# Performance work log

Measured on AMD Instinct MI355X. Metric: run time of the kernel, lower is better.

## Reference

```python
import jax, jax.numpy as jnp
import numpy as np

# ShiftedSteSign forward: binary sign (0 -> +1). STE only matters for backward.

def ste_sign(x):
    return jnp.where(x >= 0, 1.0, -1.0).astype(x.dtype)

N, D, U, E = 32768, 1024, 1024, 3  # tokens, d_in, units, kernel_estimators


def setup_inputs() -> dict:
    key = jax.random.key(0)
    kx, k0, k1, k2 = jax.random.split(key, 4)
    x = jax.random.normal(kx, (N, D), dtype=jnp.float32)
    # keras 'random_uniform' initializer default range [-0.05, 0.05]
    kernels = [jax.random.uniform(k, (D, U), jnp.float32, -0.05, 0.05) for k in (k0, k1, k2)]
    # alpha initialized as ||kernel||_1 along axis 0 divided by d_in (trainable)
    alphas = [jnp.sum(jnp.abs(kw), axis=0) / D for kw in kernels]
    return {"x": x,
            "k0": kernels[0], "k1": kernels[1], "k2": kernels[2],
            "a0": alphas[0], "a1": alphas[1], "a2": alphas[2]}


def reference(x, k0, k1, k2, a0, a1, a2):
    d = x.shape[-1]
    xq = ste_sign(x)                                   # [N, D] binary
    beta = jnp.sum(jnp.abs(x), axis=-1) / d            # [N]
    out = jnp.zeros((x.shape[0], k0.shape[1]), x.dtype)
    for kw, a in ((k0, a0), (k1, a1), (k2, a2)):
        Z = xq @ ste_sign(kw)                          # binary GEMM [N, U]
        out = out + Z * (beta[:, None] * a[None, :])   # outer-product scale
    return out
```

## Files before the change

### kernel.cpp

```cpp
#include <hip/hip_runtime.h>
#include <hip/hip_bf16.h>
#include <stdint.h>

#define N_TOK 32768
#define D_IN  1024
#define U_OUT 1024

typedef __attribute__((ext_vector_type(8))) short short8;
typedef __attribute__((ext_vector_type(4))) float f32x4;

__device__ __forceinline__ void async_copy16(const void* g, void* l) {
  __builtin_amdgcn_global_load_lds(
      (const __attribute__((address_space(1))) void*)g,
      (__attribute__((address_space(3))) void*)l,
      16, 0, 0);
}

__global__ __launch_bounds__(256) void quant_kernel(
    const float* __restrict__ x,
    unsigned short* __restrict__ xq,
    float* __restrict__ beta) {
  const int row = blockIdx.x;
  const int tid = threadIdx.x;
  const float4 v = ((const float4*)(x + (size_t)row * D_IN))[tid];

  ushort4 s;
  s.x = (v.x >= 0.f) ? 0x3F80u : 0xBF80u;
  s.y = (v.y >= 0.f) ? 0x3F80u : 0xBF80u;
  s.z = (v.z >= 0.f) ? 0x3F80u : 0xBF80u;
  s.w = (v.w >= 0.f) ? 0x3F80u : 0xBF80u;
  ((ushort4*)(xq + (size_t)row * D_IN))[tid] = s;

  float asum = fabsf(v.x) + fabsf(v.y) + fabsf(v.z) + fabsf(v.w);
  #pragma unroll
  for (int off = 32; off > 0; off >>= 1)
    asum += __shfl_down(asum, off, 64);

  __shared__ float part[4];
  if ((tid & 63) == 0) part[tid >> 6] = asum;
  __syncthreads();
  if (tid == 0)
    beta[row] = (part[0] + part[1] + part[2] + part[3]) * (1.0f / (float)D_IN);
}

__global__ __launch_bounds__(256) void wt_kernel(
    const float* __restrict__ k0, const float* __restrict__ k1,
    const float* __restrict__ k2,
    const float* __restrict__ a0, const float* __restrict__ a1,
    const float* __restrict__ a2,
    unsigned short* __restrict__ wt) {
  __shared__ float tile[64][65];
  const int d0 = blockIdx.x * 64;
  const int u0 = blockIdx.y * 64;
  const int tid = threadIdx.x;

  const int u_local = tid >> 2;
  const int dbase   = (tid & 3) * 16;
  float acc[16];
  #pragma unroll
  for (int j = 0; j < 16; j++) acc[j] = 0.f;

  const float* ks[3] = {k0, k1, k2};
  const float* as[3] = {a0, a1, a2};

  for (int e = 0; e < 3; e++) {
    __syncthreads();
    const int col   = tid & 63;
    const int rbase = tid >> 6;
    #pragma unroll
    for (int i = 0; i < 16; i++) {
      const int r = rbase + i * 4;
      tile[r][col] = ks[e][(size_t)(d0 + r) * U_OUT + (u0 + col)];
    }
    __syncthreads();
    const float a = as[e][u0 + u_local];
    #pragma unroll
    for (int j = 0; j < 16; j++) {
      const float kv = tile[dbase + j][u_local];
      acc[j] += (kv >= 0.f) ? a : -a;
    }
  }

  const size_t base = (size_t)(u0 + u_local) * D_IN + d0 + dbase;
  #pragma unroll
  for (int j = 0; j < 16; j++) {
    __hip_bfloat16 h = __float2bfloat16(acc[j]);
    wt[base + j] = *(unsigned short*)&h;
  }
}

#define BM 128
#define BN 128
#define BK 32

__global__ __launch_bounds__(256, 2) void gemm_kernel(
    const unsigned short* __restrict__ A,
    const unsigned short* __restrict__ Bt,
    const float* __restrict__ beta,
    float* __restrict__ C) {
  const int M = N_TOK, N = U_OUT, K = D_IN;
  __shared__ unsigned short As[BM * BK];
  __shared__ unsigned short Bs[BN * BK];

  const int bid = blockIdx.x;
  const int nt  = bid & 7;
  const int mt  = bid >> 3;
  const int m0  = mt * BM;
  const int n0  = nt * BN;
  (void)M;

  const int tid  = threadIdx.x;
  const int wave = tid >> 6;
  const int lane = tid & 63;
  const int wr   = wave >> 1;
  const int wc   = wave & 1;
  const int lrow = lane & 15;
  const int quad = lane >> 4;

  f32x4 acc[4][4] = {};

  for (int kk = 0; kk < K; kk += BK) {
    #pragma unroll
    for (int half = 0; half < 2; half++) {
      const int s   = tid + half * 256;
      const int row = s >> 2;
      const int c   = (s & 3) * 8;
      async_copy16(A  + (size_t)(m0 + row) * K + kk + c, As + (size_t)s * 8);
      async_copy16(Bt + (size_t)(n0 + row) * K + kk + c, Bs + (size_t)s * 8);
    }
    __syncthreads();

    short8 af[4], bf[4];
    #pragma unroll
    for (int i = 0; i < 4; i++) {
      af[i] = *(const short8*)(As + (wr * 64 + i * 16 + lrow) * BK + quad * 8);
      bf[i] = *(const short8*)(Bs + (wc * 64 + i * 16 + lrow) * BK + quad * 8);
    }
    #pragma unroll
    for (int mi = 0; mi < 4; mi++)
      #pragma unroll
      for (int ni = 0; ni < 4; ni++)
        acc[mi][ni] = __builtin_amdgcn_mfma_f32_16x16x32_bf16(
            af[mi], bf[ni], acc[mi][ni], 0, 0, 0);
    __syncthreads();
  }

  #pragma unroll
  for (int mi = 0; mi < 4; mi++) {
    #pragma unroll
    for (int r = 0; r < 4; r++) {
      const int row = m0 + wr * 64 + mi * 16 + quad * 4 + r;
      const float b = beta[row];
      #pragma unroll
      for (int ni = 0; ni < 4; ni++) {
        const int col = n0 + wc * 64 + ni * 16 + lrow;
        C[(size_t)row * N + col] = acc[mi][ni][r] * b;
      }
    }
  }
}

extern "C" void kernel_launch(void* const* d_in, const int* in_sizes, int n_in,
                              void* d_out, int out_size, void* d_ws, size_t ws_size,
                              hipStream_t stream) {
  const float* x  = (const float*)d_in[0];
  const float* k0 = (const float*)d_in[1];
  const float* k1 = (const float*)d_in[2];
  const float* k2 = (const float*)d_in[3];
  const float* a0 = (const float*)d_in[4];
  const float* a1 = (const float*)d_in[5];
  const float* a2 = (const float*)d_in[6];
  float* out = (float*)d_out;

  char* ws = (char*)d_ws;
  unsigned short* xq   = (unsigned short*)ws;
  unsigned short* wt   = (unsigned short*)(ws + (size_t)N_TOK * D_IN * 2);
  float*          beta = (float*)(ws + (size_t)N_TOK * D_IN * 2
                                     + (size_t)U_OUT * D_IN * 2);

  quant_kernel<<<N_TOK, 256, 0, stream>>>(x, xq, beta);
  wt_kernel<<<dim3(D_IN / 64, U_OUT / 64), 256, 0, stream>>>(
      k0, k1, k2, a0, a1, a2, wt);
  gemm_kernel<<<(N_TOK / BM) * (U_OUT / BN), 256, 0, stream>>>(xq, wt, beta, out);
}
```

Baseline: 349.8 us.

## Switch binary GEMM to int8 MFMA with per-column quantized folded weights

Signed activations are stored as int8 ±1, and the three scaled sign kernels are folded into one weight matrix. That matrix is quantized to int8 with a per-column scale and multiplied with the i8 MFMA (K=64 per instruction), with beta and the column scale applied in the epilogue. This halves operand bytes and doubles the MFMA rate compared with bf16. The quant kernel now handles one row per wave, and the GEMM uses an XCD-aware tile mapping. Quantizing the folded weight to 127 levels adds small rounding error relative to the exact reference, and the weight prep kernel runs on only 16 blocks.

```diff
diff --git a/kernel.cpp b/kernel.cpp
--- a/kernel.cpp
+++ b/kernel.cpp
@@ -6,8 +6,7 @@
 #define D_IN  1024
 #define U_OUT 1024
 
-typedef __attribute__((ext_vector_type(8))) short short8;
-typedef __attribute__((ext_vector_type(4))) float f32x4;
+typedef __attribute__((ext_vector_type(4))) int int32x4;
 
 __device__ __forceinline__ void async_copy16(const void* g, void* l) {
   __builtin_amdgcn_global_load_lds(
@@ -18,29 +17,30 @@
 
 __global__ __launch_bounds__(256) void quant_kernel(
     const float* __restrict__ x,
-    unsigned short* __restrict__ xq,
+    char* __restrict__ xq,
     float* __restrict__ beta) {
-  const int row = blockIdx.x;
-  const int tid = threadIdx.x;
-  const float4 v = ((const float4*)(x + (size_t)row * D_IN))[tid];
+  const int wave = threadIdx.x >> 6;
+  const int lane = threadIdx.x & 63;
+  const int row  = blockIdx.x * 4 + wave;
 
-  ushort4 s;
-  s.x = (v.x >= 0.f) ? 0x3F80u : 0xBF80u;
-  s.y = (v.y >= 0.f) ? 0x3F80u : 0xBF80u;
-  s.z = (v.z >= 0.f) ? 0x3F80u : 0xBF80u;
-  s.w = (v.w >= 0.f) ? 0x3F80u : 0xBF80u;
-  ((ushort4*)(xq + (size_t)row * D_IN))[tid] = s;
+  const float4* p = (const float4*)(x + (size_t)row * D_IN);
+  alignas(16) char sb[16];
+  float asum = 0.f;
+  #pragma unroll
+  for (int j = 0; j < 4; ++j) {
+    const float4 v = p[lane * 4 + j];
+    asum += fabsf(v.x) + fabsf(v.y) + fabsf(v.z) + fabsf(v.w);
+    sb[j * 4 + 0] = (v.x >= 0.f) ? 1 : -1;
+    sb[j * 4 + 1] = (v.y >= 0.f) ? 1 : -1;
+    sb[j * 4 + 2] = (v.z >= 0.f) ? 1 : -1;
+    sb[j * 4 + 3] = (v.w >= 0.f) ? 1 : -1;
+  }
+  *(int32x4*)(xq + (size_t)row * D_IN + lane * 16) = *(const int32x4*)sb;
 
-  float asum = fabsf(v.x) + fabsf(v.y) + fabsf(v.z) + fabsf(v.w);
   #pragma unroll
   for (int off = 32; off > 0; off >>= 1)
     asum += __shfl_down(asum, off, 64);
-
-  __shared__ float part[4];
-  if ((tid & 63) == 0) part[tid >> 6] = asum;
-  __syncthreads();
-  if (tid == 0)
-    beta[row] = (part[0] + part[1] + part[2] + part[3]) * (1.0f / (float)D_IN);
+  if (lane == 0) beta[row] = asum * (1.0f / (float)D_IN);
 }
 
 __global__ __launch_bounds__(256) void wt_kernel(
@@ -48,66 +48,69 @@
     const float* __restrict__ k2,
     const float* __restrict__ a0, const float* __restrict__ a1,
     const float* __restrict__ a2,
-    unsigned short* __restrict__ wt) {
-  __shared__ float tile[64][65];
-  const int d0 = blockIdx.x * 64;
-  const int u0 = blockIdx.y * 64;
+    char* __restrict__ wt,
+    float* __restrict__ q) {
   const int tid = threadIdx.x;
+  const int ul  = tid & 63;
+  const int dg  = tid >> 6;
+  const int u   = blockIdx.x * 64 + ul;
+  const float av0 = a0[u], av1 = a1[u], av2 = a2[u];
 
-  const int u_local = tid >> 2;
-  const int dbase   = (tid & 3) * 16;
-  float acc[16];
-  #pragma unroll
-  for (int j = 0; j < 16; j++) acc[j] = 0.f;
+  float mx = 0.f;
+  for (int j = 0; j < 256; ++j) {
+    const size_t idx = (size_t)(dg * 256 + j) * U_OUT + u;
+    const float w = (k0[idx] >= 0.f ? av0 : -av0)
+                  + (k1[idx] >= 0.f ? av1 : -av1)
+                  + (k2[idx] >= 0.f ? av2 : -av2);
+    mx = fmaxf(mx, fabsf(w));
+  }
+  __shared__ float smax[4][64];
+  smax[dg][ul] = mx;
+  __syncthreads();
+  const float m4 = fmaxf(fmaxf(smax[0][ul], smax[1][ul]),
+                         fmaxf(smax[2][ul], smax[3][ul]));
+  const float qv  = fmaxf(m4, 1e-20f) * (1.0f / 127.0f);
+  const float inv = 127.0f / fmaxf(m4, 1e-20f);
+  if (dg == 0) q[u] = qv;
 
-  const float* ks[3] = {k0, k1, k2};
-  const float* as[3] = {a0, a1, a2};
-
-  for (int e = 0; e < 3; e++) {
-    __syncthreads();
-    const int col   = tid & 63;
-    const int rbase = tid >> 6;
+  for (int c = 0; c < 16; ++c) {
+    alignas(16) char buf[16];
     #pragma unroll
-    for (int i = 0; i < 16; i++) {
-      const int r = rbase + i * 4;
-      tile[r][col] = ks[e][(size_t)(d0 + r) * U_OUT + (u0 + col)];
+    for (int j = 0; j < 16; ++j) {
+      const size_t idx = (size_t)(dg * 256 + c * 16 + j) * U_OUT + u;
+      const float w = (k0[idx] >= 0.f ? av0 : -av0)
+                    + (k1[idx] >= 0.f ? av1 : -av1)
+                    + (k2[idx] >= 0.f ? av2 : -av2);
+      int v = (int)rintf(w * inv);
+      v = v > 127 ? 127 : (v < -127 ? -127 : v);
+      buf[j] = (char)v;
     }
-    __syncthreads();
-    const float a = as[e][u0 + u_local];
-    #pragma unroll
-    for (int j = 0; j < 16; j++) {
-      const float kv = tile[dbase + j][u_local];
-      acc[j] += (kv >= 0.f) ? a : -a;
-    }
-  }
-
-  const size_t base = (size_t)(u0 + u_local) * D_IN + d0 + dbase;
-  #pragma unroll
-  for (int j = 0; j < 16; j++) {
-    __hip_bfloat16 h = __float2bfloat16(acc[j]);
-    wt[base + j] = *(unsigned short*)&h;
+    *(int32x4*)(wt + (size_t)u * D_IN + dg * 256 + c * 16) =
+        *(const int32x4*)buf;
   }
 }
 
 #define BM 128
 #define BN 128
-#define BK 32
+#define BK 64
 
 __global__ __launch_bounds__(256, 2) void gemm_kernel(
-    const unsigned short* __restrict__ A,
-    const unsigned short* __restrict__ Bt,
+    const char* __restrict__ A,
+    const char* __restrict__ Bt,
     const float* __restrict__ beta,
+    const float* __restrict__ q,
     float* __restrict__ C) {
-  const int M = N_TOK, N = U_OUT, K = D_IN;
-  __shared__ unsigned short As[BM * BK];
-  __shared__ unsigned short Bs[BN * BK];
+  const int K = D_IN, N = U_OUT;
+  __shared__ char As[BM * BK];
+  __shared__ char Bs[BN * BK];
 
   const int bid = blockIdx.x;
-  const int nt  = bid & 7;
-  const int mt  = bid >> 3;
+  const int xcd = bid & 7;
+  const int g   = bid >> 3;
+  const int mt  = xcd * 32 + (g >> 3);
+  const int nt  = g & 7;
   const int m0  = mt * BM;
   const int n0  = nt * BN;
-  (void)M;
 
   const int tid  = threadIdx.x;
   const int wave = tid >> 6;
@@ -117,30 +120,30 @@
   const int lrow = lane & 15;
   const int quad = lane >> 4;
 
-  f32x4 acc[4][4] = {};
+  int32x4 acc[4][4] = {};
 
   for (int kk = 0; kk < K; kk += BK) {
     #pragma unroll
     for (int half = 0; half < 2; half++) {
       const int s   = tid + half * 256;
       const int row = s >> 2;
-      const int c   = (s & 3) * 8;
-      async_copy16(A  + (size_t)(m0 + row) * K + kk + c, As + (size_t)s * 8);
-      async_copy16(Bt + (size_t)(n0 + row) * K + kk + c, Bs + (size_t)s * 8);
+      const int c   = (s & 3) * 16;
+      async_copy16(A  + (size_t)(m0 + row) * K + kk + c, As + (size_t)s * 16);
+      async_copy16(Bt + (size_t)(n0 + row) * K + kk + c, Bs + (size_t)s * 16);
     }
     __syncthreads();
 
-    short8 af[4], bf[4];
+    int32x4 af[4], bf[4];
     #pragma unroll
     for (int i = 0; i < 4; i++) {
-      af[i] = *(const short8*)(As + (wr * 64 + i * 16 + lrow) * BK + quad * 8);
-      bf[i] = *(const short8*)(Bs + (wc * 64 + i * 16 + lrow) * BK + quad * 8);
+      af[i] = *(const int32x4*)(As + (wr * 64 + i * 16 + lrow) * BK + quad * 16);
+      bf[i] = *(const int32x4*)(Bs + (wc * 64 + i * 16 + lrow) * BK + quad * 16);
     }
     #pragma unroll
     for (int mi = 0; mi < 4; mi++)
       #pragma unroll
       for (int ni = 0; ni < 4; ni++)
-        acc[mi][ni] = __builtin_amdgcn_mfma_f32_16x16x32_bf16(
+        acc[mi][ni] = __builtin_amdgcn_mfma_i32_16x16x64_i8(
             af[mi], bf[ni], acc[mi][ni], 0, 0, 0);
     __syncthreads();
   }
@@ -154,7 +157,7 @@
       #pragma unroll
       for (int ni = 0; ni < 4; ni++) {
         const int col = n0 + wc * 64 + ni * 16 + lrow;
-        C[(size_t)row * N + col] = acc[mi][ni][r] * b;
+        C[(size_t)row * N + col] = (float)acc[mi][ni][r] * b * q[col];
       }
     }
   }
@@ -173,13 +176,12 @@
   float* out = (float*)d_out;
 
   char* ws = (char*)d_ws;
-  unsigned short* xq   = (unsigned short*)ws;
-  unsigned short* wt   = (unsigned short*)(ws + (size_t)N_TOK * D_IN * 2);
-  float*          beta = (float*)(ws + (size_t)N_TOK * D_IN * 2
-                                     + (size_t)U_OUT * D_IN * 2);
+  char*  xq   = ws;
+  char*  wt   = ws + (size_t)N_TOK * D_IN;
+  float* q    = (float*)(wt + (size_t)U_OUT * D_IN);
+  float* beta = q + U_OUT;
 
-  quant_kernel<<<N_TOK, 256, 0, stream>>>(x, xq, beta);
-  wt_kernel<<<dim3(D_IN / 64, U_OUT / 64), 256, 0, stream>>>(
-      k0, k1, k2, a0, a1, a2, wt);
-  gemm_kernel<<<(N_TOK / BM) * (U_OUT / BN), 256, 0, stream>>>(xq, wt, beta, out);
+  quant_kernel<<<N_TOK / 4, 256, 0, stream>>>(x, xq, beta);
+  wt_kernel<<<U_OUT / 64, 256, 0, stream>>>(k0, k1, k2, a0, a1, a2, wt, q);
+  gemm_kernel<<<(N_TOK / BM) * (U_OUT / BN), 256, 0, stream>>>(xq, wt, beta, q, out);
 }
```

Measured after the change: 388.8 us. +11.2%, slower.
